# Kernel optimization log

Measured on AMD Instinct MI355X. Metric: run time of the kernel, lower is better.

## Reference

```python
import jax, jax.numpy as jnp
import numpy as np

B, EEG_D, FMRI_D, BD, H, NC = 131072, 128, 64, 128, 4, 2
HD = BD // H  # head dim = 32
EPS = 1e-5

def layernorm(x, g, b):
    m = jnp.mean(x, axis=-1, keepdims=True)
    v = jnp.var(x, axis=-1, keepdims=True)
    return (x - m) * jax.lax.rsqrt(v + EPS) * g + b

def setup_inputs() -> dict:
    key = jax.random.key(0)
    ks = jax.random.split(key, 24)
    r = lambda i, shape, s=0.05: jax.random.normal(ks[i], shape, dtype=jnp.float32) * s
    return {
        'eeg_feats': jax.random.normal(ks[0], (B, EEG_D), dtype=jnp.float32),
        'fmri_feats': jax.random.normal(ks[1], (B, FMRI_D), dtype=jnp.float32),
        # projections (weights stored [in, out])
        'We': r(2, (EEG_D, BD)), 'be': jnp.zeros((BD,)),
        'ge': jnp.ones((BD,)), 'bge': jnp.zeros((BD,)),
        'Wf': r(3, (FMRI_D, BD)), 'bf': jnp.zeros((BD,)),
        'gf': jnp.ones((BD,)), 'bgf': jnp.zeros((BD,)),
        # multihead attention
        'Wq': r(4, (BD, BD)), 'bq': jnp.zeros((BD,)),
        'Wk': r(5, (BD, BD)), 'bk': jnp.zeros((BD,)),
        'Wv': r(6, (BD, BD)), 'bv': jnp.zeros((BD,)),
        'Wo': r(7, (BD, BD)), 'bo': jnp.zeros((BD,)),
        # learned fusion
        'fusion_logits': jnp.zeros((2,)),
        'temperature': jnp.ones(()),
        # classifier
        'Wc1': r(8, (BD, BD // 2)), 'bc1': jnp.zeros((BD // 2,)),
        'gc': jnp.ones((BD // 2,)), 'bgc': jnp.zeros((BD // 2,)),
        'Wc2': r(9, (BD // 2, NC)), 'bc2': jnp.zeros((NC,)),
    }

def reference(eeg_feats, fmri_feats, We, be, ge, bge, Wf, bf, gf, bgf,
              Wq, bq, Wk, bk, Wv, bv, Wo, bo, fusion_logits, temperature,
              Wc1, bc1, gc, bgc, Wc2, bc2):
    # modality projections: Linear + LN + GELU (dropout off at eval)
    eeg_p = jax.nn.gelu(layernorm(eeg_feats @ We + be, ge, bge), approximate=False)
    fmri_p = jax.nn.gelu(layernorm(fmri_feats @ Wf + bf, gf, bgf), approximate=False)

    # cross-attention: query = eeg_p (1 token), kv = [eeg_p, fmri_p] (2 tokens)
    seq = jnp.stack([eeg_p, fmri_p], axis=1)                 # [B, 2, BD]
    q = (eeg_p @ Wq + bq).reshape(B, H, HD)                  # [B, H, HD]
    k = (seq @ Wk + bk).reshape(B, 2, H, HD)
    v = (seq @ Wv + bv).reshape(B, 2, H, HD)
    scores = jnp.einsum('bhd,bkhd->bhk', q, k) / jnp.sqrt(jnp.float32(HD))
    attn = jax.nn.softmax(scores, axis=-1)                   # [B, H, 2]
    ctx = jnp.einsum('bhk,bkhd->bhd', attn, v).reshape(B, BD)
    eeg_enh = ctx @ Wo + bo                                  # [B, BD]

    # learned temperature-scaled fusion over [eeg_enhanced, fmri_proj]
    w = jax.nn.softmax(fusion_logits / temperature, axis=0)
    fused = w[0] * eeg_enh + w[1] * fmri_p                   # [B, BD]

    # classifier: Linear + LN + ReLU + Linear
    h = jax.nn.relu(layernorm(fused @ Wc1 + bc1, gc, bgc))
    logits = h @ Wc2 + bc2                                   # [B, NC]
    return logits
```

## Files before the change

kernel.cpp:

```cpp
#include <hip/hip_runtime.h>
#include <math.h>

#define EPS 1e-5f
#define SCALE 0.17677669529663687f

#define OFF_We  0
#define OFF_Wf  16384
#define OFF_Wq  24576
#define OFF_Wk  40960
#define OFF_Wv  57344
#define OFF_Wo  73728
#define OFF_Wc1 90112
#define PACK_TOTAL 98304

#define P_BE   0
#define P_GE   128
#define P_BGE  256
#define P_BF   384
#define P_GF   512
#define P_BGF  640
#define P_BQ   768
#define P_BK   896
#define P_BV   1024
#define P_BO   1152
#define P_BC1  1280
#define P_GC   1344
#define P_BGC  1408
#define P_WC2  1472
#define P_MISC 1600
#define PARAM_N 1605

typedef __bf16 bf16x8 __attribute__((ext_vector_type(8)));
typedef float f32x4 __attribute__((ext_vector_type(4)));
typedef unsigned short ushort_t;
typedef unsigned short ushortx4 __attribute__((ext_vector_type(4)));

__device__ __forceinline__ ushort_t f2bf(float x) {
    unsigned u = __builtin_bit_cast(unsigned, x);
    u = (u + 0x7fffu + ((u >> 16) & 1u)) >> 16;
    return (ushort_t)u;
}
__device__ __forceinline__ float bf2f(ushort_t v) {
    unsigned u = ((unsigned)v) << 16;
    return __builtin_bit_cast(float, u);
}

#define DPPADD(x, ctrl) \
    ((x) + __builtin_bit_cast(float, __builtin_amdgcn_update_dpp( \
        __builtin_bit_cast(int, (x)), __builtin_bit_cast(int, (x)), (ctrl), 0xF, 0xF, false)))

__device__ __forceinline__ float rowsum16(float x) {
    x = DPPADD(x, 0x121);
    x = DPPADD(x, 0x122);
    x = DPPADD(x, 0x124);
    x = DPPADD(x, 0x128);
    return x;
}

__device__ __forceinline__ float gelu_fast(float x) {
    float x2 = x * x;
    float u = x * fmaf(0.07135481283f, x2, 1.5957691216f);
    float e = __expf(-u);
    return x * __builtin_amdgcn_rcpf(1.0f + e);
}

__global__ __launch_bounds__(256) void pack_all(
    const float* __restrict__ We, const float* __restrict__ Wf,
    const float* __restrict__ Wq, const float* __restrict__ Wk,
    const float* __restrict__ Wv, const float* __restrict__ Wo,
    const float* __restrict__ Wc1,
    const float* __restrict__ be, const float* __restrict__ ge, const float* __restrict__ bge,
    const float* __restrict__ bf, const float* __restrict__ gf, const float* __restrict__ bgf,
    const float* __restrict__ bq, const float* __restrict__ bk, const float* __restrict__ bv,
    const float* __restrict__ bo, const float* __restrict__ bc1, const float* __restrict__ gc,
    const float* __restrict__ bgc, const float* __restrict__ Wc2, const float* __restrict__ bc2,
    const float* __restrict__ fl, const float* __restrict__ temp,
    ushort_t* __restrict__ ws)
{
    int o = blockIdx.x * 256 + threadIdx.x;
    if (o < PACK_TOTAL) {
        const float* W; int K, N, base;
        if (o < OFF_Wf)        { W = We;  K = 128; N = 128; base = OFF_We; }
        else if (o < OFF_Wq)   { W = Wf;  K = 64;  N = 128; base = OFF_Wf; }
        else if (o < OFF_Wk)   { W = Wq;  K = 128; N = 128; base = OFF_Wq; }
        else if (o < OFF_Wv)   { W = Wk;  K = 128; N = 128; base = OFF_Wk; }
        else if (o < OFF_Wo)   { W = Wv;  K = 128; N = 128; base = OFF_Wv; }
        else if (o < OFF_Wc1)  { W = Wo;  K = 128; N = 128; base = OFF_Wo; }
        else                   { W = Wc1; K = 128; N = 64;  base = OFF_Wc1; }
        int e = o - base;
        int j = e & 7, l = (e >> 3) & 63, rest = e >> 9;
        int KS = K >> 5;
        int s = rest % KS, t = rest / KS;
        int k = s * 32 + ((l >> 4) << 3) + j;
        int n = (t << 4) + (l & 15);
        ws[o] = f2bf(W[k * N + n]);
        return;
    }
    int p = o - PACK_TOTAL;
    if (p >= PARAM_N) return;
    float* wsf = (float*)(ws + PACK_TOTAL);
    float v;
    if (p < 128)        v = be[p];
    else if (p < 256)   v = ge[p - 128];
    else if (p < 384)   v = bge[p - 256];
    else if (p < 512)   v = bf[p - 384];
    else if (p < 640)   v = gf[p - 512];
    else if (p < 768)   v = bgf[p - 640];
    else if (p < 896)   v = bq[p - 768];
    else if (p < 1024)  v = bk[p - 896];
    else if (p < 1152)  v = bv[p - 1024];
    else if (p < 1280)  v = bo[p - 1152];
    else if (p < 1344)  v = bc1[p - 1280];
    else if (p < 1408)  v = gc[p - 1344];
    else if (p < 1472)  v = bgc[p - 1408];
    else if (p < 1600)  v = Wc2[p - 1472];
    else if (p == 1600) v = bc2[0];
    else if (p == 1601) v = bc2[1];
    else if (p == 1602) v = fl[0];
    else if (p == 1603) v = fl[1];
    else                v = temp[0];
    wsf[p] = v;
}

template<int KS>
__device__ __forceinline__ void load_af(bf16x8 af[KS], const ushort_t* A, int lane)
{
    const int quad = lane >> 4, l16 = lane & 15;
    #pragma unroll
    for (int ks = 0; ks < KS; ++ks)
        af[ks] = *(const bf16x8*)(A + l16 * 136 + ks * 32 + quad * 8);
}

template<int KS, int NTN>
__device__ __forceinline__ void mma_lds(const bf16x8 af[KS],
    const ushort_t* sW, const float* sB, int nt0, float acc[NTN][4], int lane)
{
    const int l16 = lane & 15;
    #pragma unroll
    for (int t = 0; t < NTN; ++t) {
        float b = sB[(nt0 + t) * 16 + l16];
        f32x4 a0 = {b, b, b, b};
        #pragma unroll
        for (int ks = 0; ks < KS; ++ks) {
            bf16x8 bb = *(const bf16x8*)(sW + (((nt0 + t) * KS + ks) * 64 + lane) * 8);
            a0 = __builtin_amdgcn_mfma_f32_16x16x32_bf16(af[ks], bb, a0, 0, 0, 0);
        }
        #pragma unroll
        for (int r = 0; r < 4; ++r) acc[t][r] = a0[r];
    }
}

__global__ __launch_bounds__(256, 2) void fusion_stage(
    const float* __restrict__ eeg, const float* __restrict__ fmri,
    const ushort_t* __restrict__ ws, float* __restrict__ out)
{
    __shared__ __align__(16) ushort_t sW[16384];
    __shared__ __align__(16) float sP[1664];
    __shared__ __align__(16) ushort_t B1[4][16 * 136];
    __shared__ __align__(16) ushort_t B2[4][16 * 136];

    const int tid = threadIdx.x;
    const int wave = tid >> 6, lane = tid & 63;
    const int quad = lane >> 4, l16 = lane & 15;
    const int rowbase = blockIdx.x * 64 + wave * 16;
    ushort_t* b1 = B1[wave];
    ushort_t* b2 = B2[wave];

    {
        const float* src = (const float*)(ws + PACK_TOTAL);
        for (int i = tid; i < PARAM_N; i += 256) sP[i] = src[i];
    }

    {
        const float4* src = (const float4*)(eeg + (size_t)rowbase * 128);
        #pragma unroll
        for (int i = 0; i < 8; ++i) {
            int idx = i * 64 + lane;
            float4 v = src[idx];
            int r = idx >> 5, k4 = (idx & 31) * 4;
            *(ushortx4*)&b1[r * 136 + k4] =
                (ushortx4){f2bf(v.x), f2bf(v.y), f2bf(v.z), f2bf(v.w)};
        }
        const float4* srcf = (const float4*)(fmri + (size_t)rowbase * 64);
        #pragma unroll
        for (int i = 0; i < 4; ++i) {
            int idx = i * 64 + lane;
            float4 v = srcf[idx];
            int r = idx >> 4, k4 = (idx & 15) * 4;
            *(ushortx4*)&b2[r * 136 + k4] =
                (ushortx4){f2bf(v.x), f2bf(v.y), f2bf(v.z), f2bf(v.w)};
        }
    }

    auto stageW = [&](int offU, int nUsh) {
        __syncthreads();
        const uint4* g = (const uint4*)(ws + offU);
        uint4* d = (uint4*)sW;
        int n16 = nUsh >> 3;
        for (int i = tid; i < n16; i += 256) d[i] = g[i];
        __syncthreads();
    };

    float meanS[4], rstdS[4];

    stageW(OFF_We, 16384);
    {
        bf16x8 afR[4]; load_af<4>(afR, b1, lane);
        float acc[8][4];
        mma_lds<4, 8>(afR, sW, sP + P_BE, 0, acc, lane);
        #pragma unroll
        for (int r = 0; r < 4; ++r) {
            float s = 0.f, ss = 0.f;
            #pragma unroll
            for (int nt = 0; nt < 8; ++nt) { float x = acc[nt][r]; s += x; ss = fmaf(x, x, ss); }
            s = rowsum16(s); ss = rowsum16(ss);
            float m = s * (1.f / 128.f);
            meanS[r] = m;
            rstdS[r] = rsqrtf(ss * (1.f / 128.f) - m * m + EPS);
        }
        #pragma unroll
        for (int nt = 0; nt < 8; ++nt) {
            float g = sP[P_GE + nt * 16 + l16], bb = sP[P_BGE + nt * 16 + l16];
            #pragma unroll
            for (int r = 0; r < 4; ++r) {
                float x = (acc[nt][r] - meanS[r]) * rstdS[r] * g + bb;
                b1[(quad * 4 + r) * 136 + nt * 16 + l16] = f2bf(gelu_fast(x));
            }
        }
    }

    stageW(OFF_Wf, 8192);
    {
        bf16x8 afR[2]; load_af<2>(afR, b2, lane);
        float acc[8][4];
        mma_lds<2, 8>(afR, sW, sP + P_BF, 0, acc, lane);
        #pragma unroll
        for (int r = 0; r < 4; ++r) {
            float s = 0.f, ss = 0.f;
            #pragma unroll
            for (int nt = 0; nt < 8; ++nt) { float x = acc[nt][r]; s += x; ss = fmaf(x, x, ss); }
            s = rowsum16(s); ss = rowsum16(ss);
            float m = s * (1.f / 128.f);
            meanS[r] = m;
            rstdS[r] = rsqrtf(ss * (1.f / 128.f) - m * m + EPS);
        }
        #pragma unroll
        for (int nt = 0; nt < 8; ++nt) {
            float g = sP[P_GF + nt * 16 + l16], bb = sP[P_BGF + nt * 16 + l16];
            #pragma unroll
            for (int r = 0; r < 4; ++r) {
                float x = (acc[nt][r] - meanS[r]) * rstdS[r] * g + bb;
                b2[(quad * 4 + r) * 136 + nt * 16 + l16] = f2bf(gelu_fast(x));
            }
        }
    }

    bf16x8 afE[4]; load_af<4>(afE, b1, lane);
    bf16x8 afF[4]; load_af<4>(afF, b2, lane);

    stageW(OFF_Wq, 16384);
    float q[8][4];
    mma_lds<4, 8>(afE, sW, sP + P_BQ, 0, q, lane);

    stageW(OFF_Wk, 16384);
    float a0v[4][4];
    {
        float p0a[4][4], p1a[4][4];
        #pragma unroll
        for (int h = 0; h < 4; ++h)
            #pragma unroll
            for (int r = 0; r < 4; ++r) { p0a[h][r] = 0.f; p1a[h][r] = 0.f; }
        #pragma unroll
        for (int nt = 0; nt < 8; ++nt) {
            float b = sP[P_BK + nt * 16 + l16];
            f32x4 e = {b, b, b, b}, f = {b, b, b, b};
            #pragma unroll
            for (int ks = 0; ks < 4; ++ks) {
                bf16x8 bb = *(const bf16x8*)(sW + ((nt * 4 + ks) * 64 + lane) * 8);
                e = __builtin_amdgcn_mfma_f32_16x16x32_bf16(afE[ks], bb, e, 0, 0, 0);
                f = __builtin_amdgcn_mfma_f32_16x16x32_bf16(afF[ks], bb, f, 0, 0, 0);
            }
            int h = nt >> 1;
            #pragma unroll
            for (int r = 0; r < 4; ++r) {
                p0a[h][r] = fmaf(q[nt][r], e[r], p0a[h][r]);
                p1a[h][r] = fmaf(q[nt][r], f[r], p1a[h][r]);
            }
        }
        #pragma unroll
        for (int h = 0; h < 4; ++h)
            #pragma unroll
            for (int r = 0; r < 4; ++r) {
                float p0 = rowsum16(p0a[h][r]);
                float p1 = rowsum16(p1a[h][r]);
                float s0 = p0 * SCALE, s1 = p1 * SCALE;
                float mx = fmaxf(s0, s1);
                float e0 = __expf(s0 - mx), e1 = __expf(s1 - mx);
                a0v[h][r] = e0 * __builtin_amdgcn_rcpf(e0 + e1);
            }
    }

    stageW(OFF_Wv, 16384);
    #pragma unroll
    for (int nt = 0; nt < 8; ++nt) {
        float b = sP[P_BV + nt * 16 + l16];
        f32x4 e = {b, b, b, b}, f = {b, b, b, b};
        #pragma unroll
        for (int ks = 0; ks < 4; ++ks) {
            bf16x8 bb = *(const bf16x8*)(sW + ((nt * 4 + ks) * 64 + lane) * 8);
            e = __builtin_amdgcn_mfma_f32_16x16x32_bf16(afE[ks], bb, e, 0, 0, 0);
            f = __builtin_amdgcn_mfma_f32_16x16x32_bf16(afF[ks], bb, f, 0, 0, 0);
        }
        int h = nt >> 1;
        #pragma unroll
        for (int r = 0; r < 4; ++r) {
            float a0 = a0v[h][r];
            float c0 = a0 * e[r] + (1.0f - a0) * f[r];
            b1[(quad * 4 + r) * 136 + nt * 16 + l16] = f2bf(c0);
        }
    }

    stageW(OFF_Wo, 16384);
    {
        bf16x8 afC[4]; load_af<4>(afC, b1, lane);
        float acc[8][4];
        mma_lds<4, 8>(afC, sW, sP + P_BO, 0, acc, lane);
        float t = sP[P_MISC + 4];
        float l0 = sP[P_MISC + 2] / t, l1 = sP[P_MISC + 3] / t;
        float mx = fmaxf(l0, l1);
        float ee0 = __expf(l0 - mx), ee1 = __expf(l1 - mx);
        float w0 = ee0 / (ee0 + ee1), w1 = 1.0f - w0;
        #pragma unroll
        for (int nt = 0; nt < 8; ++nt)
            #pragma unroll
            for (int r = 0; r < 4; ++r) {
                int off = (quad * 4 + r) * 136 + nt * 16 + l16;
                float fp = bf2f(b2[off]);
                b1[off] = f2bf(w0 * acc[nt][r] + w1 * fp);
            }
    }

    stageW(OFF_Wc1, 8192);
    {
        bf16x8 afU[4]; load_af<4>(afU, b1, lane);
        float accH[4][4];
        mma_lds<4, 4>(afU, sW, sP + P_BC1, 0, accH, lane);
        #pragma unroll
        for (int r = 0; r < 4; ++r) {
            float s = 0.f, ss = 0.f;
            #pragma unroll
            for (int nt = 0; nt < 4; ++nt) { float x = accH[nt][r]; s += x; ss = fmaf(x, x, ss); }
            s = rowsum16(s); ss = rowsum16(ss);
            float m = s * (1.f / 64.f);
            meanS[r] = m;
            rstdS[r] = rsqrtf(ss * (1.f / 64.f) - m * m + EPS);
        }
        #pragma unroll
        for (int nt = 0; nt < 4; ++nt) {
            float g = sP[P_GC + nt * 16 + l16], bb = sP[P_BGC + nt * 16 + l16];
            #pragma unroll
            for (int r = 0; r < 4; ++r) {
                float x = (accH[nt][r] - meanS[r]) * rstdS[r] * g + bb;
                accH[nt][r] = fmaxf(x, 0.0f);
            }
        }
        float w2v[4][2];
        #pragma unroll
        for (int nt = 0; nt < 4; ++nt) {
            float2 w = *(const float2*)&sP[P_WC2 + (nt * 16 + l16) * 2];
            w2v[nt][0] = w.x; w2v[nt][1] = w.y;
        }
        float o0c = sP[P_MISC + 0], o1c = sP[P_MISC + 1];
        #pragma unroll
        for (int r = 0; r < 4; ++r) {
            float p0 = 0.f, p1 = 0.f;
            #pragma unroll
            for (int nt = 0; nt < 4; ++nt) {
                float hv = accH[nt][r];
                p0 = fmaf(hv, w2v[nt][0], p0);
                p1 = fmaf(hv, w2v[nt][1], p1);
            }
            p0 = rowsum16(p0); p1 = rowsum16(p1);
            if (l16 == 0) {
                int row = rowbase + quad * 4 + r;
                float2 o; o.x = p0 + o0c; o.y = p1 + o1c;
                *(float2*)&out[row * 2] = o;
            }
        }
    }
}

extern "C" void kernel_launch(void* const* d_in, const int* in_sizes, int n_in,
                              void* d_out, int out_size, void* d_ws, size_t ws_size,
                              hipStream_t stream) {
    const float* eeg  = (const float*)d_in[0];
    const float* fmri = (const float*)d_in[1];
    const float* We   = (const float*)d_in[2];
    const float* be   = (const float*)d_in[3];
    const float* ge   = (const float*)d_in[4];
    const float* bge  = (const float*)d_in[5];
    const float* Wf   = (const float*)d_in[6];
    const float* bf   = (const float*)d_in[7];
    const float* gf   = (const float*)d_in[8];
    const float* bgf  = (const float*)d_in[9];
    const float* Wq   = (const float*)d_in[10];
    const float* bq   = (const float*)d_in[11];
    const float* Wk   = (const float*)d_in[12];
    const float* bk   = (const float*)d_in[13];
    const float* Wv   = (const float*)d_in[14];
    const float* bv   = (const float*)d_in[15];
    const float* Wo   = (const float*)d_in[16];
    const float* bo   = (const float*)d_in[17];
    const float* fl   = (const float*)d_in[18];
    const float* temp = (const float*)d_in[19];
    const float* Wc1  = (const float*)d_in[20];
    const float* bc1  = (const float*)d_in[21];
    const float* gc   = (const float*)d_in[22];
    const float* bgc  = (const float*)d_in[23];
    const float* Wc2  = (const float*)d_in[24];
    const float* bc2  = (const float*)d_in[25];
    float* out = (float*)d_out;
    ushort_t* ws = (ushort_t*)d_ws;

    int packThreads = PACK_TOTAL + 2048;
    hipLaunchKernelGGL(pack_all, dim3((packThreads + 255) / 256), dim3(256), 0, stream,
                       We, Wf, Wq, Wk, Wv, Wo, Wc1,
                       be, ge, bge, bf, gf, bgf, bq, bk, bv, bo,
                       bc1, gc, bgc, Wc2, bc2, fl, temp, ws);

    int B = in_sizes[0] / 128;
    int grid = B / 64;
    hipLaunchKernelGGL(fusion_stage, dim3(grid), dim3(256), 0, stream,
                       eeg, fmri, ws, out);
}
```

Before: 233.8 us.

## Prefetch next stage weights into registers and simplify two-key softmax to sigmoid

```diff
diff --git a/kernel.cpp b/kernel.cpp
--- a/kernel.cpp
+++ b/kernel.cpp
@@ -122,6 +122,24 @@
     wsf[p] = v;
 }
 
+template<int NR>
+__device__ __forceinline__ void pf_load(const ushort_t* __restrict__ ws, int offU,
+                                        int tid, uint4* regs)
+{
+    const uint4* g = (const uint4*)(ws + offU);
+    #pragma unroll
+    for (int i = 0; i < NR; ++i) regs[i] = g[tid + i * 256];
+}
+template<int NR>
+__device__ __forceinline__ void pf_commit(ushort_t* sW, int tid, const uint4* regs)
+{
+    __syncthreads();
+    uint4* d = (uint4*)sW;
+    #pragma unroll
+    for (int i = 0; i < NR; ++i) d[tid + i * 256] = regs[i];
+    __syncthreads();
+}
+
 template<int KS>
 __device__ __forceinline__ void load_af(bf16x8 af[KS], const ushort_t* A, int lane)
 {
@@ -166,6 +184,9 @@
     ushort_t* b1 = B1[wave];
     ushort_t* b2 = B2[wave];
 
+    uint4 pf[8];
+    pf_load<8>(ws, OFF_We, tid, pf);
+
     {
         const float* src = (const float*)(ws + PACK_TOTAL);
         for (int i = tid; i < PARAM_N; i += 256) sP[i] = src[i];
@@ -192,18 +213,10 @@
         }
     }
 
-    auto stageW = [&](int offU, int nUsh) {
-        __syncthreads();
-        const uint4* g = (const uint4*)(ws + offU);
-        uint4* d = (uint4*)sW;
-        int n16 = nUsh >> 3;
-        for (int i = tid; i < n16; i += 256) d[i] = g[i];
-        __syncthreads();
-    };
-
     float meanS[4], rstdS[4];
 
-    stageW(OFF_We, 16384);
+    pf_commit<8>(sW, tid, pf);
+    pf_load<4>(ws, OFF_Wf, tid, pf);
     {
         bf16x8 afR[4]; load_af<4>(afR, b1, lane);
         float acc[8][4];
@@ -229,7 +242,8 @@
         }
     }
 
-    stageW(OFF_Wf, 8192);
+    pf_commit<4>(sW, tid, pf);
+    pf_load<8>(ws, OFF_Wq, tid, pf);
     {
         bf16x8 afR[2]; load_af<2>(afR, b2, lane);
         float acc[8][4];
@@ -258,22 +272,23 @@
     bf16x8 afE[4]; load_af<4>(afE, b1, lane);
     bf16x8 afF[4]; load_af<4>(afF, b2, lane);
 
-    stageW(OFF_Wq, 16384);
+    pf_commit<8>(sW, tid, pf);
+    pf_load<8>(ws, OFF_Wk, tid, pf);
     float q[8][4];
     mma_lds<4, 8>(afE, sW, sP + P_BQ, 0, q, lane);
 
-    stageW(OFF_Wk, 16384);
+    pf_commit<8>(sW, tid, pf);
+    pf_load<8>(ws, OFF_Wv, tid, pf);
     float a0v[4][4];
     {
-        float p0a[4][4], p1a[4][4];
+        float pd[4][4];
         #pragma unroll
         for (int h = 0; h < 4; ++h)
             #pragma unroll
-            for (int r = 0; r < 4; ++r) { p0a[h][r] = 0.f; p1a[h][r] = 0.f; }
+            for (int r = 0; r < 4; ++r) pd[h][r] = 0.f;
         #pragma unroll
         for (int nt = 0; nt < 8; ++nt) {
-            float b = sP[P_BK + nt * 16 + l16];
-            f32x4 e = {b, b, b, b}, f = {b, b, b, b};
+            f32x4 e = {0.f, 0.f, 0.f, 0.f}, f = {0.f, 0.f, 0.f, 0.f};
             #pragma unroll
             for (int ks = 0; ks < 4; ++ks) {
                 bf16x8 bb = *(const bf16x8*)(sW + ((nt * 4 + ks) * 64 + lane) * 8);
@@ -282,25 +297,20 @@
             }
             int h = nt >> 1;
             #pragma unroll
+            for (int r = 0; r < 4; ++r)
+                pd[h][r] = fmaf(q[nt][r], e[r] - f[r], pd[h][r]);
+        }
+        #pragma unroll
+        for (int h = 0; h < 4; ++h)
+            #pragma unroll
             for (int r = 0; r < 4; ++r) {
-                p0a[h][r] = fmaf(q[nt][r], e[r], p0a[h][r]);
-                p1a[h][r] = fmaf(q[nt][r], f[r], p1a[h][r]);
-            }
-        }
-        #pragma unroll
-        for (int h = 0; h < 4; ++h)
-            #pragma unroll
-            for (int r = 0; r < 4; ++r) {
-                float p0 = rowsum16(p0a[h][r]);
-                float p1 = rowsum16(p1a[h][r]);
-                float s0 = p0 * SCALE, s1 = p1 * SCALE;
-                float mx = fmaxf(s0, s1);
-                float e0 = __expf(s0 - mx), e1 = __expf(s1 - mx);
-                a0v[h][r] = e0 * __builtin_amdgcn_rcpf(e0 + e1);
-            }
-    }
-
-    stageW(OFF_Wv, 16384);
+                float d = rowsum16(pd[h][r]) * SCALE;
+                a0v[h][r] = __builtin_amdgcn_rcpf(1.0f + __expf(-d));
+            }
+    }
+
+    pf_commit<8>(sW, tid, pf);
+    pf_load<8>(ws, OFF_Wo, tid, pf);
     #pragma unroll
     for (int nt = 0; nt < 8; ++nt) {
         float b = sP[P_BV + nt * 16 + l16];
@@ -320,16 +330,16 @@
         }
     }
 
-    stageW(OFF_Wo, 16384);
+    pf_commit<8>(sW, tid, pf);
+    pf_load<4>(ws, OFF_Wc1, tid, pf);
     {
         bf16x8 afC[4]; load_af<4>(afC, b1, lane);
         float acc[8][4];
         mma_lds<4, 8>(afC, sW, sP + P_BO, 0, acc, lane);
         float t = sP[P_MISC + 4];
-        float l0 = sP[P_MISC + 2] / t, l1 = sP[P_MISC + 3] / t;
-        float mx = fmaxf(l0, l1);
-        float ee0 = __expf(l0 - mx), ee1 = __expf(l1 - mx);
-        float w0 = ee0 / (ee0 + ee1), w1 = 1.0f - w0;
+        float dl = (sP[P_MISC + 2] - sP[P_MISC + 3]) / t;
+        float w0 = __builtin_amdgcn_rcpf(1.0f + __expf(-dl));
+        float w1 = 1.0f - w0;
         #pragma unroll
         for (int nt = 0; nt < 8; ++nt)
             #pragma unroll
@@ -340,7 +350,7 @@
             }
     }
 
-    stageW(OFF_Wc1, 8192);
+    pf_commit<4>(sW, tid, pf);
     {
         bf16x8 afU[4]; load_af<4>(afU, b1, lane);
         float accH[4][4];
```

Measured after the change: 291.1 us. 24.5% more time.
